# Performance work log

Measured on AMD Instinct MI355X. Metric: run time of the kernel, lower is better.

Reference implementation:

```python
import jax, jax.numpy as jnp
import numpy as np

D_MODEL = 1024
N_HEADS = 16
HEAD_DIM = D_MODEL // N_HEADS
N_MEM = 16
EPS = 1e-5
ROPE_THETA = 10000.0


def layernorm(x, g, b):
    mu = jnp.mean(x, axis=-1, keepdims=True)
    var = jnp.mean(jnp.square(x - mu), axis=-1, keepdims=True)
    return (x - mu) * jax.lax.rsqrt(var + EPS) * g + b


def rope_cos_sin(seq_len, head_dim, dtype):
    inv_freq = 1.0 / (ROPE_THETA ** (jnp.arange(0, head_dim, 2, dtype=jnp.float32) / head_dim))
    pos = jnp.arange(seq_len, dtype=jnp.float32)
    freqs = pos[:, None] * inv_freq[None, :]            # [S, hd/2]
    emb = jnp.concatenate([freqs, freqs], axis=-1)       # [S, hd]
    return jnp.cos(emb).astype(dtype), jnp.sin(emb).astype(dtype)


def rotate_half(x):
    x1, x2 = jnp.split(x, 2, axis=-1)
    return jnp.concatenate([-x2, x1], axis=-1)


def setup_inputs() -> dict:
    key = jax.random.key(0)
    ks = jax.random.split(key, 8)
    B, T, D = 2, 2048, D_MODEL
    x = jax.random.normal(ks[0], (B, T, D), dtype=jnp.float32)
    memory_tokens = jax.random.normal(ks[1], (1, N_MEM, D), dtype=jnp.float32) * 0.02
    s = 1.0 / np.sqrt(D)
    qkv_w = jax.random.uniform(ks[2], (3 * D, D), minval=-s, maxval=s, dtype=jnp.float32)
    qkv_b = jax.random.uniform(ks[3], (3 * D,), minval=-s, maxval=s, dtype=jnp.float32)
    out_w = jax.random.uniform(ks[4], (D, D), minval=-s, maxval=s, dtype=jnp.float32)
    out_b = jax.random.uniform(ks[5], (D,), minval=-s, maxval=s, dtype=jnp.float32)
    norm_g = jnp.ones((D,), jnp.float32)
    norm_b = jnp.zeros((D,), jnp.float32)
    normm_g = jnp.ones((D,), jnp.float32)
    normm_b = jnp.zeros((D,), jnp.float32)
    return {"x": x, "memory_tokens": memory_tokens, "qkv_w": qkv_w, "qkv_b": qkv_b,
            "out_w": out_w, "out_b": out_b, "norm_g": norm_g, "norm_b": norm_b,
            "normm_g": normm_g, "normm_b": normm_b}


def reference(x, memory_tokens, qkv_w, qkv_b, out_w, out_b, norm_g, norm_b, normm_g, normm_b):
    B, T, D = x.shape
    S = N_MEM + T
    residual = x
    x_norm = layernorm(x, norm_g, norm_b)
    mem = layernorm(jnp.broadcast_to(memory_tokens, (B, N_MEM, D)), normm_g, normm_b)
    xm = jnp.concatenate([mem, x_norm], axis=1)                # [B, S, D]
    qkv = xm @ qkv_w.T + qkv_b                                 # [B, S, 3D]
    qkv = qkv.reshape(B, S, 3, N_HEADS, HEAD_DIM)
    q = jnp.transpose(qkv[:, :, 0], (0, 2, 1, 3))              # [B, H, S, hd]
    k = jnp.transpose(qkv[:, :, 1], (0, 2, 1, 3))
    v = jnp.transpose(qkv[:, :, 2], (0, 2, 1, 3))
    cos, sin = rope_cos_sin(S, HEAD_DIM, x.dtype)              # [S, hd]
    q = q * cos + rotate_half(q) * sin
    k = k * cos + rotate_half(k) * sin
    scale = 1.0 / np.sqrt(HEAD_DIM)
    scores = jnp.einsum("bhqd,bhkd->bhqk", q, k) * scale       # [B, H, S, S]
    causal = jnp.tril(jnp.ones((S, S), dtype=bool))
    scores = jnp.where(causal, scores, jnp.finfo(scores.dtype).min)
    attn = jax.nn.softmax(scores, axis=-1)
    out = jnp.einsum("bhqk,bhkd->bhqd", attn, v)               # [B, H, S, hd]
    out = jnp.transpose(out, (0, 2, 1, 3)).reshape(B, S, D)
    out = out @ out_w.T + out_b
    out = out[:, N_MEM:, :]
    return residual + out
```

## Files before the change

kernel.cpp:

```cpp
#include <hip/hip_runtime.h>
#include <cstdint>


using bf16 = __bf16;
typedef __attribute__((ext_vector_type(8))) __bf16 bf16x8;
typedef __attribute__((ext_vector_type(4))) __bf16 bf16x4;
typedef __attribute__((ext_vector_type(4))) float floatx4;

#define MFMA16(a, b, c) __builtin_amdgcn_mfma_f32_16x16x32_bf16(a, b, c, 0, 0, 0)

constexpr int SV = 2064;
constexpr int SP = 2112;
constexpr float LOG2_THETA = 13.287712379549449f;

__device__ __forceinline__ bool dt_is_bf16(const void* p) {
  return *(const uint32_t*)p == 0x3F803F80u;
}

struct f8 { float v[8]; };

__device__ __forceinline__ f8 load8(const void* p, size_t idx, bool bf) {
  f8 r;
  if (bf) {
    bf16x8 t = *(const bf16x8*)((const bf16*)p + idx);
#pragma unroll
    for (int j = 0; j < 8; ++j) r.v[j] = (float)t[j];
  } else {
    float4 a = *(const float4*)((const float*)p + idx);
    float4 b = *(const float4*)((const float*)p + idx + 4);
    r.v[0] = a.x; r.v[1] = a.y; r.v[2] = a.z; r.v[3] = a.w;
    r.v[4] = b.x; r.v[5] = b.y; r.v[6] = b.z; r.v[7] = b.w;
  }
  return r;
}

__device__ __forceinline__ float ld1(const void* p, size_t idx, bool bf) {
  return bf ? (float)((const bf16*)p)[idx] : ((const float*)p)[idx];
}

__device__ __forceinline__ void load16_to_lds(const bf16* gptr, bf16* lptr) {
  auto* g = reinterpret_cast<const __attribute__((address_space(1))) uint32_t*>(
      reinterpret_cast<uintptr_t>(gptr));
  auto* l = reinterpret_cast<__attribute__((address_space(3))) uint32_t*>(
      reinterpret_cast<uintptr_t>(lptr));
  __builtin_amdgcn_global_load_lds(g, l, 16, 0, 0);
}

__global__ __launch_bounds__(256) void conv_w(
    const void* __restrict__ W, const void* __restrict__ flagp,
    bf16* __restrict__ dst) {
  const bool bf = dt_is_bf16(flagp);
  const size_t i = ((size_t)blockIdx.x * 256 + threadIdx.x) * 8;
  const f8 v = load8(W, i, bf);
  bf16x8 o;
#pragma unroll
  for (int j = 0; j < 8; ++j) o[j] = (bf16)v.v[j];
  *(bf16x8*)&dst[i] = o;
}

__global__ __launch_bounds__(256) void rope_tab(float2* __restrict__ tab) {
  const int i = blockIdx.x * 256 + threadIdx.x;
  const int pos = i >> 5, f = i & 31;
  const float ang = (float)pos * exp2f((float)f * (-LOG2_THETA / 32.0f));
  float c, s;
  sincosf(ang, &c, &s);
  tab[i] = make_float2(c, s);
}

__global__ __launch_bounds__(256) void ln_all(
    const void* __restrict__ x, const void* __restrict__ mem,
    const void* __restrict__ ng, const void* __restrict__ nb,
    const void* __restrict__ mg, const void* __restrict__ mb,
    bf16* __restrict__ mem16, bf16* __restrict__ xln) {
  const bool bf = dt_is_bf16(ng);
  const int t = threadIdx.x, wid = t >> 6, lane = t & 63;
  const int row = blockIdx.x * 4 + wid;
  const void *src, *g, *bb;
  size_t soff;
  bf16* out;
  if (row < 16) {
    src = mem; soff = (size_t)row * 1024; g = mg; bb = mb;
    out = mem16 + (size_t)row * 1024;
  } else {
    src = x; soff = (size_t)(row - 16) * 1024; g = ng; bb = nb;
    out = xln + (size_t)(row - 16) * 1024;
  }
  const f8 v0 = load8(src, soff + lane * 8, bf);
  const f8 v1 = load8(src, soff + 512 + lane * 8, bf);
  float sum = 0.f, sq = 0.f;
#pragma unroll
  for (int j = 0; j < 8; ++j) { sum += v0.v[j]; sq += v0.v[j] * v0.v[j]; }
#pragma unroll
  for (int j = 0; j < 8; ++j) { sum += v1.v[j]; sq += v1.v[j] * v1.v[j]; }
#pragma unroll
  for (int off = 1; off < 64; off <<= 1) {
    sum += __shfl_xor(sum, off);
    sq += __shfl_xor(sq, off);
  }
  const float mu = sum * (1.0f / 1024.0f);
  const float var = sq * (1.0f / 1024.0f) - mu * mu;
  const float rstd = rsqrtf(var + 1e-5f);
  const f8 g0 = load8(g, lane * 8, bf), g1 = load8(g, 512 + lane * 8, bf);
  const f8 b0 = load8(bb, lane * 8, bf), b1 = load8(bb, 512 + lane * 8, bf);
  bf16x8 o0, o1;
#pragma unroll
  for (int j = 0; j < 8; ++j) {
    o0[j] = (bf16)((v0.v[j] - mu) * rstd * g0.v[j] + b0.v[j]);
    o1[j] = (bf16)((v1.v[j] - mu) * rstd * g1.v[j] + b1.v[j]);
  }
  *(bf16x8*)&out[lane * 8] = o0;
  *(bf16x8*)&out[512 + lane * 8] = o1;
}

__global__ __launch_bounds__(512, 1) void gemm0_rope(
    const bf16* __restrict__ mem16, const bf16* __restrict__ xln,
    const bf16* __restrict__ Wqb, const void* __restrict__ bias,
    const void* __restrict__ flagp, const float2* __restrict__ rtab,
    bf16* __restrict__ Qg, bf16* __restrict__ Kg, bf16* __restrict__ Vg) {
  const bool bf = dt_is_bf16(flagp);
  __shared__ bf16 SH[65536];
  const int t = threadIdx.x;
  const int row0 = blockIdx.x * 256;
  const int col0 = blockIdx.y * 256;
  const int wid = t >> 6, lane = t & 63, lr = lane & 15, lg = lane >> 4;
  const int wm = wid >> 2, wn = wid & 3;
  const int xorv = (lr & 7) << 3;

  const int coff = (((t & 7) ^ ((t >> 3) & 7)) << 3);
  const bf16* aptr[4];
  const bf16* bptr[4];
#pragma unroll
  for (int s = 0; s < 4; ++s) {
    int g = row0 + s * 64 + (t >> 3);
    if (g > 4127) g = 4127;
    const int b2 = (g >= SV) ? 1 : 0;
    const int ss = g - b2 * SV;
    const bf16* ap = (ss < 16) ? (mem16 + (size_t)ss * 1024)
                               : (xln + ((size_t)(b2 * 2048 + ss - 16)) * 1024);
    aptr[s] = ap + coff;
    bptr[s] = Wqb + (size_t)(col0 + s * 64 + (t >> 3)) * 1024 + coff;
  }

  const int ldsbase = (t & ~63) * 8;
  auto STAGE = [&](int bufi, int k0) {
    bf16* Ld = SH + bufi * 32768;
#pragma unroll
    for (int s = 0; s < 4; ++s)
      load16_to_lds(aptr[s] + k0, Ld + s * 4096 + ldsbase);
#pragma unroll
    for (int s = 0; s < 4; ++s)
      load16_to_lds(bptr[s] + k0, Ld + 16384 + s * 4096 + ldsbase);
  };

  floatx4 acc[8][4] = {};
  STAGE(0, 0);
  STAGE(1, 64);

  for (int kt = 0; kt < 16; ++kt) {
    const int cur = kt & 1;
    if (kt < 15)
      asm volatile("s_waitcnt vmcnt(8)" ::: "memory");
    else
      asm volatile("s_waitcnt vmcnt(0)" ::: "memory");
    __builtin_amdgcn_s_barrier();
    __builtin_amdgcn_sched_barrier(0);
    const bf16* Ab = SH + cur * 32768;
    const bf16* Bb = Ab + 16384;
    bf16x8 a0[8], b0[4], a1[8], b1[4];
#pragma unroll
    for (int mi = 0; mi < 8; ++mi)
      a0[mi] = *(const bf16x8*)&Ab[(wm * 128 + mi * 16 + lr) * 64 + ((lg * 8) ^ xorv)];
#pragma unroll
    for (int ni = 0; ni < 4; ++ni)
      b0[ni] = *(const bf16x8*)&Bb[(wn * 64 + ni * 16 + lr) * 64 + ((lg * 8) ^ xorv)];
    __builtin_amdgcn_s_setprio(1);
#pragma unroll
    for (int mi = 0; mi < 8; ++mi)
#pragma unroll
      for (int ni = 0; ni < 4; ++ni)
        acc[mi][ni] = MFMA16(a0[mi], b0[ni], acc[mi][ni]);
    __builtin_amdgcn_s_setprio(0);
#pragma unroll
    for (int mi = 0; mi < 8; ++mi)
      a1[mi] = *(const bf16x8*)&Ab[(wm * 128 + mi * 16 + lr) * 64 + ((32 + lg * 8) ^ xorv)];
#pragma unroll
    for (int ni = 0; ni < 4; ++ni)
      b1[ni] = *(const bf16x8*)&Bb[(wn * 64 + ni * 16 + lr) * 64 + ((32 + lg * 8) ^ xorv)];
    __builtin_amdgcn_sched_barrier(0);
    asm volatile("s_waitcnt lgkmcnt(0)" ::: "memory");
    __builtin_amdgcn_s_barrier();
    __builtin_amdgcn_sched_barrier(0);
    if (kt < 14) STAGE(cur, (kt + 2) * 64);
    __builtin_amdgcn_s_setprio(1);
#pragma unroll
    for (int mi = 0; mi < 8; ++mi)
#pragma unroll
      for (int ni = 0; ni < 4; ++ni)
        acc[mi][ni] = MFMA16(a1[mi], b1[ni], acc[mi][ni]);
    __builtin_amdgcn_s_setprio(0);
  }

  const int colbase = col0 + wn * 64;
  const int part = colbase >> 10;
  const int h = (colbase >> 6) & 15;
  const int row0w = row0 + wm * 128;

  if (part == 2) {
#pragma unroll
    for (int mi = 0; mi < 8; ++mi) {
      const int gq = row0w + mi * 16 + lg * 4;
      if (gq >= 2 * SV) continue;
      const int b2 = (gq >= SV) ? 1 : 0;
      const int pos = gq - b2 * SV;
      const size_t hb = (size_t)(b2 * 16 + h) * 64;
#pragma unroll
      for (int ni = 0; ni < 4; ++ni) {
        const int d = ni * 16 + lr;
        const float bc = ld1(bias, colbase + ni * 16 + lr, bf);
        bf16x4 vv;
#pragma unroll
        for (int r = 0; r < 4; ++r) vv[r] = (bf16)(acc[mi][ni][r] + bc);
        *(bf16x4*)&Vg[(hb + d) * SP + pos] = vv;
      }
    }
  } else {
    bf16* Dst = (part == 0) ? Qg : Kg;
    const float qs = (part == 0) ? 0.125f : 1.0f;
    float bv[4];
#pragma unroll
    for (int a = 0; a < 4; ++a) bv[a] = ld1(bias, colbase + a * 16 + lr, bf);
#pragma unroll
    for (int mi = 0; mi < 8; ++mi) {
#pragma unroll
      for (int r = 0; r < 4; ++r) {
        const int g = row0w + mi * 16 + lg * 4 + r;
        if (g >= 2 * SV) continue;
        const int b2 = (g >= SV) ? 1 : 0;
        const int pos = g - b2 * SV;
        bf16* drow = Dst + ((size_t)(b2 * 16 + h) * SP + pos) * 64;
#pragma unroll
        for (int a = 0; a < 2; ++a) {
          const float2 cs = rtab[pos * 32 + a * 16 + lr];
          const float vlo = (acc[mi][a][r] + bv[a]) * qs;
          const float vhi = (acc[mi][a + 2][r] + bv[a + 2]) * qs;
          drow[a * 16 + lr] = (bf16)(vlo * cs.x - vhi * cs.y);
          drow[32 + a * 16 + lr] = (bf16)(vhi * cs.x + vlo * cs.y);
        }
      }
    }
  }
}

__global__ __launch_bounds__(256) void flash3(
    const bf16* __restrict__ Qg, const bf16* __restrict__ Kg,
    const bf16* __restrict__ Vg, bf16* __restrict__ attn_out) {
  const int qt = 32 - blockIdx.x;
  const int bh = blockIdx.y;
  const int b = bh >> 4, h = bh & 15;
  const bf16* Qb = Qg + (size_t)bh * SP * 64;
  const bf16* Kb = Kg + (size_t)bh * SP * 64;
  const bf16* Vb = Vg + (size_t)bh * 64 * SP;

  const int t = threadIdx.x;
  const int wid = t >> 6, lane = t & 63, lr = lane & 15, lg = lane >> 4;
  const int qw0 = qt * 64 + wid * 16;

  __shared__ bf16 Ks[64 * 72];
  __shared__ bf16 Vt[64 * 64];
  __shared__ bf16 Ps[4][16 * 72];

  const int qs = qw0 + lr;
  bf16x8 qf0{}, qf1{};
  if (qs < SV) {
    qf0 = *(const bf16x8*)&Qb[(size_t)qs * 64 + lg * 8];
    qf1 = *(const bf16x8*)&Qb[(size_t)qs * 64 + 32 + lg * 8];
  }

  floatx4 o[4] = {};
  float lpart[4] = {};

  const int kr = t >> 2;
  const int kc = (t & 3) * 16;
  const int vd = t >> 2;
  const int vg0 = t & 3;
  const int vswz = ((vd & 7) ^ ((vd >> 4) & 3)) << 3;

  bf16x8 kA, kB, vA, vB;
  kA = *(const bf16x8*)&Kb[(size_t)kr * 64 + kc];
  kB = *(const bf16x8*)&Kb[(size_t)kr * 64 + kc + 8];
  vA = *(const bf16x8*)&Vb[(size_t)vd * SP + vg0 * 8];
  vB = *(const bf16x8*)&Vb[(size_t)vd * SP + (vg0 + 4) * 8];

  for (int kt = 0; kt <= qt; ++kt) {
    const int k0 = kt * 64;
    __syncthreads();
    *(bf16x8*)&Ks[kr * 72 + kc] = kA;
    *(bf16x8*)&Ks[kr * 72 + kc + 8] = kB;
    *(bf16x8*)&Vt[vd * 64 + ((vg0 << 3) ^ vswz)] = vA;
    *(bf16x8*)&Vt[vd * 64 + (((vg0 + 4) << 3) ^ vswz)] = vB;
    __syncthreads();
    if (kt < qt) {
      const int kn = k0 + 64;
      kA = *(const bf16x8*)&Kb[(size_t)(kn + kr) * 64 + kc];
      kB = *(const bf16x8*)&Kb[(size_t)(kn + kr) * 64 + kc + 8];
      vA = *(const bf16x8*)&Vb[(size_t)vd * SP + kn + vg0 * 8];
      vB = *(const bf16x8*)&Vb[(size_t)vd * SP + kn + (vg0 + 4) * 8];
    }

    floatx4 c[4] = {};
#pragma unroll
    for (int j2 = 0; j2 < 4; ++j2) {
      const bf16x8 kfa = *(const bf16x8*)&Ks[(j2 * 16 + lr) * 72 + lg * 8];
      const bf16x8 kfb = *(const bf16x8*)&Ks[(j2 * 16 + lr) * 72 + 32 + lg * 8];
      c[j2] = MFMA16(qf0, kfa, c[j2]);
      c[j2] = MFMA16(qf1, kfb, c[j2]);
    }

    const bool nm = (k0 + 63 > qw0);
#pragma unroll
    for (int r = 0; r < 4; ++r) {
      const int row = qw0 + lg * 4 + r;
      bf16* psr = &Ps[wid][(lg * 4 + r) * 72];
      float ls = 0.f;
#pragma unroll
      for (int j2 = 0; j2 < 4; ++j2) {
        float s = c[j2][r];
        if (nm && (k0 + j2 * 16 + lr > row)) s = -1e30f;
        const float p = __expf(s);
        ls += p;
        psr[j2 * 16 + lr] = (bf16)p;
      }
      lpart[r] += ls;
    }
    asm volatile("s_waitcnt lgkmcnt(0)" ::: "memory");
#pragma unroll
    for (int cc = 0; cc < 2; ++cc) {
      const bf16x8 pf = *(const bf16x8*)&Ps[wid][lr * 72 + cc * 32 + lg * 8];
#pragma unroll
      for (int dt = 0; dt < 4; ++dt) {
        const int key8 = (cc * 32 + lg * 8) ^ ((((lr & 7) ^ dt)) << 3);
        const bf16x8 vf = *(const bf16x8*)&Vt[(dt * 16 + lr) * 64 + key8];
        o[dt] = MFMA16(pf, vf, o[dt]);
      }
    }
  }

#pragma unroll
  for (int r = 0; r < 4; ++r) {
    float l = lpart[r];
    l += __shfl_xor(l, 1);
    l += __shfl_xor(l, 2);
    l += __shfl_xor(l, 4);
    l += __shfl_xor(l, 8);
    const int s = qw0 + lg * 4 + r;
    if (s < 16 || s >= SV) continue;
    const float inv = 1.0f / l;
    const size_t rowoff = ((size_t)(b * 2048 + s - 16)) * 1024 + h * 64;
#pragma unroll
    for (int dt = 0; dt < 4; ++dt)
      attn_out[rowoff + dt * 16 + lr] = (bf16)(o[dt][r] * inv);
  }
}

__global__ __launch_bounds__(256) void gemm1_proj(
    const bf16* __restrict__ A, const bf16* __restrict__ Wob,
    const void* __restrict__ bias, const void* __restrict__ x,
    const void* __restrict__ flagp, void* __restrict__ outp) {
  const bool bf = dt_is_bf16(flagp);
  __shared__ bf16 As[128 * 32];
  __shared__ bf16 Bs[128 * 32];
  const int t = threadIdx.x;
  const int row0 = blockIdx.x * 128;
  const int col0 = blockIdx.y * 128;
  const int wid = t >> 6, lane = t & 63, lr = lane & 15, lg = lane >> 4;
  const int wrow = (wid >> 1) * 64, wcol = (wid & 1) * 64;
  floatx4 acc[4][4] = {};

  const bf16* agp[2];
  const bf16* bgp[2];
#pragma unroll
  for (int c = 0; c < 2; ++c) {
    const int tt = c * 256 + t;
    agp[c] = A + (size_t)(row0 + (tt >> 2)) * 1024 + (tt & 3) * 8;
    bgp[c] = Wob + (size_t)(col0 + (tt >> 2)) * 1024 + (tt & 3) * 8;
  }

  for (int k0 = 0; k0 < 1024; k0 += 32) {
    __syncthreads();
#pragma unroll
    for (int c = 0; c < 2; ++c) {
      const int tt = c * 256 + t;
      load16_to_lds(agp[c] + k0, &As[(tt & ~63) * 8]);
      load16_to_lds(bgp[c] + k0, &Bs[(tt & ~63) * 8]);
    }
    __syncthreads();
    bf16x8 af[4], bfr[4];
#pragma unroll
    for (int i = 0; i < 4; ++i) {
      af[i] = *(const bf16x8*)&As[(wrow + i * 16 + lr) * 32 + lg * 8];
      bfr[i] = *(const bf16x8*)&Bs[(wcol + i * 16 + lr) * 32 + lg * 8];
    }
#pragma unroll
    for (int mi = 0; mi < 4; ++mi)
#pragma unroll
      for (int ni = 0; ni < 4; ++ni)
        acc[mi][ni] = MFMA16(af[mi], bfr[ni], acc[mi][ni]);
  }

#pragma unroll
  for (int mi = 0; mi < 4; ++mi) {
#pragma unroll
    for (int r = 0; r < 4; ++r) {
      const int row = row0 + wrow + mi * 16 + lg * 4 + r;
#pragma unroll
      for (int ni = 0; ni < 4; ++ni) {
        const int col = col0 + wcol + ni * 16 + lr;
        const size_t idx = (size_t)row * 1024 + col;
        const float v = acc[mi][ni][r] + ld1(bias, col, bf) + ld1(x, idx, bf);
        if (bf)
          ((bf16*)outp)[idx] = (bf16)v;
        else
          ((float*)outp)[idx] = v;
      }
    }
  }
}

extern "C" void kernel_launch(void* const* d_in, const int* in_sizes, int n_in,
                              void* d_out, int out_size, void* d_ws, size_t ws_size,
                              hipStream_t stream) {
  const void* x = d_in[0];
  const void* mem = d_in[1];
  const void* qkvw = d_in[2];
  const void* qkvb = d_in[3];
  const void* outw = d_in[4];
  const void* outb = d_in[5];
  const void* ng = d_in[6];
  const void* nb = d_in[7];
  const void* mg = d_in[8];
  const void* mb = d_in[9];

  char* ws = (char*)d_ws;
  bf16* mem16 = (bf16*)(ws);
  bf16* xln = (bf16*)(ws + 32768);
  bf16* Qg = (bf16*)(ws + 8421376);
  bf16* Kg = (bf16*)(ws + 17072128);
  bf16* Vg = (bf16*)(ws + 25722880);
  bf16* Wqb = (bf16*)(ws + 34373632);
  bf16* Wob = (bf16*)(ws + 40665088);
  bf16* attn = xln;
  float2* rtab = (float2*)Wob;

  conv_w<<<1536, 256, 0, stream>>>(qkvw, ng, Wqb);
  ln_all<<<1028, 256, 0, stream>>>(x, mem, ng, nb, mg, mb, mem16, xln);
  rope_tab<<<258, 256, 0, stream>>>(rtab);
  gemm0_rope<<<dim3(17, 12), 512, 0, stream>>>(mem16, xln, Wqb, qkvb, ng, rtab,
                                               Qg, Kg, Vg);
  conv_w<<<512, 256, 0, stream>>>(outw, ng, Wob);
  flash3<<<dim3(33, 32), 256, 0, stream>>>(Qg, Kg, Vg, attn);
  gemm1_proj<<<dim3(32, 8), 256, 0, stream>>>(attn, Wob, outb, x, ng, d_out);
}
```

Baseline: 232.0 us.

## Double-buffer K/V tiles and keep P in registers via permlane swaps in flash attention

After: 221.3 us. -4.6%, faster.

```diff
diff --git a/kernel.cpp b/kernel.cpp
--- a/kernel.cpp
+++ b/kernel.cpp
@@ -44,6 +44,12 @@
   auto* l = reinterpret_cast<__attribute__((address_space(3))) uint32_t*>(
       reinterpret_cast<uintptr_t>(lptr));
   __builtin_amdgcn_global_load_lds(g, l, 16, 0, 0);
+}
+
+__device__ __forceinline__ unsigned cvtpk_bf16(float lo, float hi) {
+  unsigned r;
+  asm("v_cvt_pk_bf16_f32 %0, %1, %2" : "=v"(r) : "v"(lo), "v"(hi));
+  return r;
 }
 
 __global__ __launch_bounds__(256) void conv_w(
@@ -225,7 +231,7 @@
     }
   } else {
     bf16* Dst = (part == 0) ? Qg : Kg;
-    const float qs = (part == 0) ? 0.125f : 1.0f;
+    const float qs = (part == 0) ? 0.18033688011f : 1.0f;
     float bv[4];
 #pragma unroll
     for (int a = 0; a < 4; ++a) bv[a] = ld1(bias, colbase + a * 16 + lr, bf);
@@ -264,20 +270,19 @@
   const int t = threadIdx.x;
   const int wid = t >> 6, lane = t & 63, lr = lane & 15, lg = lane >> 4;
   const int qw0 = qt * 64 + wid * 16;
-
-  __shared__ bf16 Ks[64 * 72];
-  __shared__ bf16 Vt[64 * 64];
-  __shared__ bf16 Ps[4][16 * 72];
-
-  const int qs = qw0 + lr;
+  const int q = qw0 + lr;
+
+  __shared__ bf16 Ks[2][64 * 72];
+  __shared__ bf16 Vt[2][64 * 64];
+
   bf16x8 qf0{}, qf1{};
-  if (qs < SV) {
-    qf0 = *(const bf16x8*)&Qb[(size_t)qs * 64 + lg * 8];
-    qf1 = *(const bf16x8*)&Qb[(size_t)qs * 64 + 32 + lg * 8];
+  if (q < SV) {
+    qf0 = *(const bf16x8*)&Qb[(size_t)q * 64 + lg * 8];
+    qf1 = *(const bf16x8*)&Qb[(size_t)q * 64 + 32 + lg * 8];
   }
 
   floatx4 o[4] = {};
-  float lpart[4] = {};
+  float lsum = 0.f;
 
   const int kr = t >> 2;
   const int kc = (t & 3) * 16;
@@ -291,70 +296,106 @@
   vA = *(const bf16x8*)&Vb[(size_t)vd * SP + vg0 * 8];
   vB = *(const bf16x8*)&Vb[(size_t)vd * SP + (vg0 + 4) * 8];
 
+  *(bf16x8*)&Ks[0][kr * 72 + kc] = kA;
+  *(bf16x8*)&Ks[0][kr * 72 + kc + 8] = kB;
+  *(bf16x8*)&Vt[0][vd * 64 + ((vg0 << 3) ^ vswz)] = vA;
+  *(bf16x8*)&Vt[0][vd * 64 + (((vg0 + 4) << 3) ^ vswz)] = vB;
+  if (qt >= 1) {
+    kA = *(const bf16x8*)&Kb[(size_t)(64 + kr) * 64 + kc];
+    kB = *(const bf16x8*)&Kb[(size_t)(64 + kr) * 64 + kc + 8];
+    vA = *(const bf16x8*)&Vb[(size_t)vd * SP + 64 + vg0 * 8];
+    vB = *(const bf16x8*)&Vb[(size_t)vd * SP + 64 + (vg0 + 4) * 8];
+  }
+  asm volatile("s_waitcnt lgkmcnt(0)" ::: "memory");
+  __builtin_amdgcn_s_barrier();
+  __builtin_amdgcn_sched_barrier(0);
+
   for (int kt = 0; kt <= qt; ++kt) {
+    const int cur = kt & 1;
     const int k0 = kt * 64;
-    __syncthreads();
-    *(bf16x8*)&Ks[kr * 72 + kc] = kA;
-    *(bf16x8*)&Ks[kr * 72 + kc + 8] = kB;
-    *(bf16x8*)&Vt[vd * 64 + ((vg0 << 3) ^ vswz)] = vA;
-    *(bf16x8*)&Vt[vd * 64 + (((vg0 + 4) << 3) ^ vswz)] = vB;
-    __syncthreads();
     if (kt < qt) {
-      const int kn = k0 + 64;
-      kA = *(const bf16x8*)&Kb[(size_t)(kn + kr) * 64 + kc];
-      kB = *(const bf16x8*)&Kb[(size_t)(kn + kr) * 64 + kc + 8];
-      vA = *(const bf16x8*)&Vb[(size_t)vd * SP + kn + vg0 * 8];
-      vB = *(const bf16x8*)&Vb[(size_t)vd * SP + kn + (vg0 + 4) * 8];
+      const int nb2 = cur ^ 1;
+      *(bf16x8*)&Ks[nb2][kr * 72 + kc] = kA;
+      *(bf16x8*)&Ks[nb2][kr * 72 + kc + 8] = kB;
+      *(bf16x8*)&Vt[nb2][vd * 64 + ((vg0 << 3) ^ vswz)] = vA;
+      *(bf16x8*)&Vt[nb2][vd * 64 + (((vg0 + 4) << 3) ^ vswz)] = vB;
+      if (kt + 1 < qt) {
+        const int kn = k0 + 128;
+        kA = *(const bf16x8*)&Kb[(size_t)(kn + kr) * 64 + kc];
+        kB = *(const bf16x8*)&Kb[(size_t)(kn + kr) * 64 + kc + 8];
+        vA = *(const bf16x8*)&Vb[(size_t)vd * SP + kn + vg0 * 8];
+        vB = *(const bf16x8*)&Vb[(size_t)vd * SP + kn + (vg0 + 4) * 8];
+      }
     }
 
     floatx4 c[4] = {};
+    __builtin_amdgcn_s_setprio(1);
 #pragma unroll
     for (int j2 = 0; j2 < 4; ++j2) {
-      const bf16x8 kfa = *(const bf16x8*)&Ks[(j2 * 16 + lr) * 72 + lg * 8];
-      const bf16x8 kfb = *(const bf16x8*)&Ks[(j2 * 16 + lr) * 72 + 32 + lg * 8];
-      c[j2] = MFMA16(qf0, kfa, c[j2]);
-      c[j2] = MFMA16(qf1, kfb, c[j2]);
-    }
+      const bf16x8 kfa = *(const bf16x8*)&Ks[cur][(j2 * 16 + lr) * 72 + lg * 8];
+      const bf16x8 kfb = *(const bf16x8*)&Ks[cur][(j2 * 16 + lr) * 72 + 32 + lg * 8];
+      c[j2] = MFMA16(kfa, qf0, c[j2]);
+      c[j2] = MFMA16(kfb, qf1, c[j2]);
+    }
+    __builtin_amdgcn_s_setprio(0);
 
     const bool nm = (k0 + 63 > qw0);
-#pragma unroll
-    for (int r = 0; r < 4; ++r) {
-      const int row = qw0 + lg * 4 + r;
-      bf16* psr = &Ps[wid][(lg * 4 + r) * 72];
-      float ls = 0.f;
-#pragma unroll
-      for (int j2 = 0; j2 < 4; ++j2) {
-        float s = c[j2][r];
-        if (nm && (k0 + j2 * 16 + lr > row)) s = -1e30f;
-        const float p = __expf(s);
-        ls += p;
-        psr[j2 * 16 + lr] = (bf16)p;
-      }
-      lpart[r] += ls;
-    }
-    asm volatile("s_waitcnt lgkmcnt(0)" ::: "memory");
+    float pr[4][4];
+#pragma unroll
+    for (int j2 = 0; j2 < 4; ++j2) {
+#pragma unroll
+      for (int rr = 0; rr < 4; ++rr) {
+        float s = c[j2][rr];
+        if (nm && (k0 + j2 * 16 + lg * 4 + rr > q)) s = -1e30f;
+        float p;
+        asm("v_exp_f32 %0, %1" : "=v"(p) : "v"(s));
+        lsum += p;
+        pr[j2][rr] = p;
+      }
+    }
+
+    unsigned paw[2][4];
 #pragma unroll
     for (int cc = 0; cc < 2; ++cc) {
-      const bf16x8 pf = *(const bf16x8*)&Ps[wid][lr * 72 + cc * 32 + lg * 8];
+#pragma unroll
+      for (int p_ = 0; p_ < 2; ++p_) {
+        unsigned a = cvtpk_bf16(pr[2 * cc][2 * p_], pr[2 * cc][2 * p_ + 1]);
+        unsigned b2 = cvtpk_bf16(pr[2 * cc + 1][2 * p_], pr[2 * cc + 1][2 * p_ + 1]);
+        asm("v_permlane32_swap_b32 %0, %1" : "+v"(a), "+v"(b2));
+        asm("v_permlane16_swap_b32 %0, %1" : "+v"(a), "+v"(b2));
+        paw[cc][p_] = a;
+        paw[cc][2 + p_] = b2;
+      }
+    }
+
+    __builtin_amdgcn_s_setprio(1);
+#pragma unroll
+    for (int cc = 0; cc < 2; ++cc) {
+      union { unsigned w[4]; bf16x8 v; } pu;
+      pu.w[0] = paw[cc][0]; pu.w[1] = paw[cc][1];
+      pu.w[2] = paw[cc][2]; pu.w[3] = paw[cc][3];
 #pragma unroll
       for (int dt = 0; dt < 4; ++dt) {
         const int key8 = (cc * 32 + lg * 8) ^ ((((lr & 7) ^ dt)) << 3);
-        const bf16x8 vf = *(const bf16x8*)&Vt[(dt * 16 + lr) * 64 + key8];
-        o[dt] = MFMA16(pf, vf, o[dt]);
-      }
-    }
-  }
-
+        const bf16x8 vf = *(const bf16x8*)&Vt[cur][(dt * 16 + lr) * 64 + key8];
+        o[dt] = MFMA16(pu.v, vf, o[dt]);
+      }
+    }
+    __builtin_amdgcn_s_setprio(0);
+    asm volatile("s_waitcnt lgkmcnt(0)" ::: "memory");
+    __builtin_amdgcn_s_barrier();
+    __builtin_amdgcn_sched_barrier(0);
+  }
+
+  float l = lsum;
+  l += __shfl_xor(l, 16);
+  l += __shfl_xor(l, 32);
 #pragma unroll
   for (int r = 0; r < 4; ++r) {
-    float l = lpart[r];
-    l += __shfl_xor(l, 1);
-    l += __shfl_xor(l, 2);
-    l += __shfl_xor(l, 4);
-    l += __shfl_xor(l, 8);
+    const float lv = __shfl(l, lg * 4 + r);
     const int s = qw0 + lg * 4 + r;
     if (s < 16 || s >= SV) continue;
-    const float inv = 1.0f / l;
+    const float inv = 1.0f / lv;
     const size_t rowoff = ((size_t)(b * 2048 + s - 16)) * 1024 + h * 64;
 #pragma unroll
     for (int dt = 0; dt < 4; ++dt)
```
